# Kernel optimization log

Hardware: AMD Instinct MI355X
Metric: run time of the kernel (lower is better)

## Reference

```python
import jax, jax.numpy as jnp
import numpy as np

EPS = 1e-06
C = 2.0 + EPS

def setup_inputs() -> dict:
    key = jax.random.key(0)
    k1, k2 = jax.random.split(key)
    B, H, D, M, R = 65536, 16, 64, 32, 2
    x = jax.random.normal(k1, (B, H * D), dtype=jnp.float32)
    omega = jax.random.normal(k2, (R, H, D, M), dtype=jnp.float32)
    nodes, weights = np.polynomial.laguerre.laggauss(R)
    quad_nodes = jnp.asarray(nodes, dtype=jnp.float32) / C
    quad_weights = jnp.asarray(weights, dtype=jnp.float32) / C
    return {"x": x, "omega": omega, "quad_nodes": quad_nodes, "quad_weights": quad_weights}

def reference(x, omega, quad_nodes, quad_weights):
    B = x.shape[0]
    R, H, D, M = omega.shape
    inv_sqrt_m = 1.0 / float(M) ** 0.5
    # reshape to heads and normalize each head vector to unit length
    xr = x.reshape(B, H, D)
    norm = jnp.linalg.norm(xr, axis=-1, keepdims=True)
    x_norm = xr / jnp.clip(norm, 1e-06)
    # small projection: contract over head_dim (d=64)
    proj = jnp.einsum('bhd,rhdm->rbhm', x_norm, omega)  # [R,B,H,M]
    poly_feat = proj ** 2 * inv_sqrt_m
    s_vals = quad_nodes.reshape(-1, 1, 1, 1)  # [R,1,1,1]
    sqrt_2s = jnp.sqrt(2.0 * jnp.clip(s_vals, 0.0))
    exp_arg = jnp.clip(proj * sqrt_2s - s_vals, -10.0, 10.0)
    prf_feat = jnp.exp(exp_arg) * inv_sqrt_m
    sq_weights = jnp.sqrt(jnp.clip(quad_weights.reshape(-1, 1, 1, 1), 0.0))
    fused = poly_feat * prf_feat * sq_weights  # [R,B,H,M]
    fused = fused.transpose(1, 2, 0, 3)  # [B,H,R,M]
    return fused.reshape(B, -1)
```

## Files before the change

kernel.cpp:

```cpp
#include <hip/hip_runtime.h>
#include <hip/hip_bf16.h>
#include <math.h>


#define HH 16
#define DD 64
#define MM 32
#define RR 2
#define NN (RR*MM)
#define TILE_B 512
#define NST (TILE_B/64)

using short8  = __attribute__((ext_vector_type(8))) short;
using floatx4 = __attribute__((ext_vector_type(4))) float;

__device__ __forceinline__ short bf16_hi(float v) {
    __hip_bfloat16 b = __float2bfloat16(v);
    return __builtin_bit_cast(short, b);
}
__device__ __forceinline__ float bf16_f(short s) {
    return __uint_as_float(((unsigned)(unsigned short)s) << 16);
}

__global__ __launch_bounds__(256, 5)
void slay_mfma_kernel(const float* __restrict__ x,
                      const float* __restrict__ omega,
                      const float* __restrict__ qn,
                      const float* __restrict__ qw,
                      float* __restrict__ out)
{
    __shared__ short lds_hi[NN * DD];
    __shared__ short lds_lo[NN * DD];
    __shared__ float lds_oc[4][16 * 64];

    const int tid  = threadIdx.x;
    const int lane = tid & 63;
    const int wv   = tid >> 6;
    const int h    = blockIdx.x & (HH - 1);
    const int tile = blockIdx.x >> 4;

    const int mrow = lane & 15;
    const int g    = lane >> 4;

    #pragma unroll
    for (int i = 0; i < (RR * DD * MM) / 256; ++i) {
        int e  = i * 256 + tid;
        int rr = e >> 11;
        int d  = (e >> 5) & (DD - 1);
        int m  = e & (MM - 1);
        float v = omega[((size_t)(rr * HH + h) * DD + d) * MM + m];
        short hi = bf16_hi(v);
        short lo = bf16_hi(v - bf16_f(hi));
        int n   = rr * MM + m;
        int byt = (d * 2) ^ ((n & 7) << 4);
        *(short*)((char*)lds_hi + n * (DD * 2) + byt) = hi;
        *(short*)((char*)lds_lo + n * (DD * 2) + byt) = lo;
    }
    __syncthreads();

    const float sn[2]  = { qn[0], qn[1] };
    const float s2s[2] = { sqrtf(2.f * fmaxf(sn[0], 0.f)), sqrtf(2.f * fmaxf(sn[1], 0.f)) };
    const float cr[2]  = { sqrtf(fmaxf(qw[0], 0.f)) * (1.f / MM),
                           sqrtf(fmaxf(qw[1], 0.f)) * (1.f / MM) };

    const int sw = (mrow & 7) << 4;
    char* const wb = (char*)lds_oc[wv];

    const float* xr0 = x + (size_t)(tile * TILE_B + wv * 16 + mrow) * (HH * DD) + h * DD;

    #pragma unroll
    for (int st = 0; st < NST; ++st) {
        const float* xr = xr0 + (size_t)st * 64 * (HH * DD);
        const int b_base = tile * TILE_B + st * 64 + wv * 16;

        float xv[16];
        *(float4*)(xv + 0)  = *(const float4*)(xr + g * 8);
        *(float4*)(xv + 4)  = *(const float4*)(xr + g * 8 + 4);
        *(float4*)(xv + 8)  = *(const float4*)(xr + 32 + g * 8);
        *(float4*)(xv + 12) = *(const float4*)(xr + 32 + g * 8 + 4);

        float ss = 0.f;
        #pragma unroll
        for (int j = 0; j < 16; ++j) ss = fmaf(xv[j], xv[j], ss);
        ss += __shfl_xor(ss, 16, 64);
        ss += __shfl_xor(ss, 32, 64);
        const float rnorm = 1.0f / fmaxf(sqrtf(ss), 1e-6f);

        short8 x_hi[2], x_lo[2];
        #pragma unroll
        for (int kc = 0; kc < 2; ++kc)
            #pragma unroll
            for (int j = 0; j < 8; ++j) {
                float v  = xv[kc * 8 + j];
                short hi = bf16_hi(v);
                x_hi[kc][j] = hi;
                x_lo[kc][j] = bf16_hi(v - bf16_f(hi));
            }

        #pragma unroll
        for (int nt = 0; nt < 4; ++nt) {
            const char* rh = (const char*)lds_hi + (nt * 16 + mrow) * (DD * 2);
            const char* rl = (const char*)lds_lo + (nt * 16 + mrow) * (DD * 2);
            const int k0 = (g * 16) ^ sw;
            const int k1 = (64 + g * 16) ^ sw;
            short8 oh0 = *(const short8*)(rh + k0);
            short8 oh1 = *(const short8*)(rh + k1);
            short8 ol0 = *(const short8*)(rl + k0);
            short8 ol1 = *(const short8*)(rl + k1);

            floatx4 acc = {0.f, 0.f, 0.f, 0.f};
            acc = __builtin_amdgcn_mfma_f32_16x16x32_bf16(oh0, x_hi[0], acc, 0, 0, 0);
            acc = __builtin_amdgcn_mfma_f32_16x16x32_bf16(oh1, x_hi[1], acc, 0, 0, 0);
            acc = __builtin_amdgcn_mfma_f32_16x16x32_bf16(oh0, x_lo[0], acc, 0, 0, 0);
            acc = __builtin_amdgcn_mfma_f32_16x16x32_bf16(oh1, x_lo[1], acc, 0, 0, 0);
            acc = __builtin_amdgcn_mfma_f32_16x16x32_bf16(ol0, x_hi[0], acc, 0, 0, 0);
            acc = __builtin_amdgcn_mfma_f32_16x16x32_bf16(ol1, x_hi[1], acc, 0, 0, 0);

            const int r = nt >> 1;
            floatx4 res;
            #pragma unroll
            for (int q = 0; q < 4; ++q) {
                float proj = acc[q] * rnorm;
                float ea = fmaf(proj, s2s[r], -sn[r]);
                ea = fminf(fmaxf(ea, -10.f), 10.f);
                res[q] = proj * proj * __expf(ea) * cr[r];
            }
            *(floatx4*)(wb + mrow * 256 + ((nt * 64 + g * 16) ^ sw)) = res;
        }

        #pragma unroll
        for (int i = 0; i < 4; ++i) {
            const int row = i * 4 + g;
            const int col = (mrow) * 16;
            floatx4 v = *(const floatx4*)(wb + row * 256 + (col ^ ((row & 7) << 4)));
            float* op = out + (size_t)(b_base + row) * (HH * NN) + h * NN + mrow * 4;
            __builtin_nontemporal_store(v, (floatx4*)op);
        }
    }
}

extern "C" void kernel_launch(void* const* d_in, const int* in_sizes, int n_in,
                              void* d_out, int out_size, void* d_ws, size_t ws_size,
                              hipStream_t stream) {
    const float* x     = (const float*)d_in[0];
    const float* omega = (const float*)d_in[1];
    const float* qn    = (const float*)d_in[2];
    const float* qw    = (const float*)d_in[3];
    float* out = (float*)d_out;

    const int B = in_sizes[0] / (HH * DD);
    dim3 grid((B / TILE_B) * HH);
    dim3 block(256);

    slay_mfma_kernel<<<grid, block, 0, stream>>>(x, omega, qn, qw, out);
}
```

Measured before the change: 89.47 us.

## Process two heads per block for wider contiguous loads and stores

Each block now handles a pair of adjacent heads instead of one. It stages omega for both heads in LDS and loads 128 contiguous x floats per row. Each output row segment written is 512 bytes instead of 256, which improves coalescing of global reads and writes and halves the grid size. The cost is double the LDS footprint, more registers per thread, and a lower launch_bounds occupancy hint (2 instead of 5), which may reduce latency hiding.

```diff
diff --git a/kernel.cpp b/kernel.cpp
--- a/kernel.cpp
+++ b/kernel.cpp
@@ -22,39 +22,41 @@
     return __uint_as_float(((unsigned)(unsigned short)s) << 16);
 }
 
-__global__ __launch_bounds__(256, 5)
+__global__ __launch_bounds__(256, 2)
 void slay_mfma_kernel(const float* __restrict__ x,
                       const float* __restrict__ omega,
                       const float* __restrict__ qn,
                       const float* __restrict__ qw,
                       float* __restrict__ out)
 {
-    __shared__ short lds_hi[NN * DD];
-    __shared__ short lds_lo[NN * DD];
-    __shared__ float lds_oc[4][16 * 64];
+    __shared__ short lds_hi[2][NN * DD];
+    __shared__ short lds_lo[2][NN * DD];
+    __shared__ float lds_oc[4][16 * 128];
 
     const int tid  = threadIdx.x;
     const int lane = tid & 63;
     const int wv   = tid >> 6;
-    const int h    = blockIdx.x & (HH - 1);
-    const int tile = blockIdx.x >> 4;
+    const int hp   = blockIdx.x & (HH / 2 - 1);
+    const int tile = blockIdx.x >> 3;
+    const int h0   = hp * 2;
 
     const int mrow = lane & 15;
     const int g    = lane >> 4;
 
     #pragma unroll
-    for (int i = 0; i < (RR * DD * MM) / 256; ++i) {
+    for (int i = 0; i < (2 * RR * DD * MM) / 256; ++i) {
         int e  = i * 256 + tid;
-        int rr = e >> 11;
+        int hh = e >> 12;
+        int rr = (e >> 11) & 1;
         int d  = (e >> 5) & (DD - 1);
         int m  = e & (MM - 1);
-        float v = omega[((size_t)(rr * HH + h) * DD + d) * MM + m];
+        float v = omega[((size_t)(rr * HH + h0 + hh) * DD + d) * MM + m];
         short hi = bf16_hi(v);
         short lo = bf16_hi(v - bf16_f(hi));
         int n   = rr * MM + m;
         int byt = (d * 2) ^ ((n & 7) << 4);
-        *(short*)((char*)lds_hi + n * (DD * 2) + byt) = hi;
-        *(short*)((char*)lds_lo + n * (DD * 2) + byt) = lo;
+        *(short*)((char*)lds_hi[hh] + n * (DD * 2) + byt) = hi;
+        *(short*)((char*)lds_lo[hh] + n * (DD * 2) + byt) = lo;
     }
     __syncthreads();
 
@@ -66,74 +68,85 @@
     const int sw = (mrow & 7) << 4;
     char* const wb = (char*)lds_oc[wv];
 
-    const float* xr0 = x + (size_t)(tile * TILE_B + wv * 16 + mrow) * (HH * DD) + h * DD;
+    const float* xr0 = x + (size_t)(tile * TILE_B + wv * 16 + mrow) * (HH * DD) + h0 * DD;
 
     #pragma unroll
     for (int st = 0; st < NST; ++st) {
         const float* xr = xr0 + (size_t)st * 64 * (HH * DD);
         const int b_base = tile * TILE_B + st * 64 + wv * 16;
 
-        float xv[16];
+        float xv[32];
         *(float4*)(xv + 0)  = *(const float4*)(xr + g * 8);
         *(float4*)(xv + 4)  = *(const float4*)(xr + g * 8 + 4);
         *(float4*)(xv + 8)  = *(const float4*)(xr + 32 + g * 8);
         *(float4*)(xv + 12) = *(const float4*)(xr + 32 + g * 8 + 4);
+        *(float4*)(xv + 16) = *(const float4*)(xr + 64 + g * 8);
+        *(float4*)(xv + 20) = *(const float4*)(xr + 64 + g * 8 + 4);
+        *(float4*)(xv + 24) = *(const float4*)(xr + 96 + g * 8);
+        *(float4*)(xv + 28) = *(const float4*)(xr + 96 + g * 8 + 4);
 
-        float ss = 0.f;
+        float rnorm[2];
         #pragma unroll
-        for (int j = 0; j < 16; ++j) ss = fmaf(xv[j], xv[j], ss);
-        ss += __shfl_xor(ss, 16, 64);
-        ss += __shfl_xor(ss, 32, 64);
-        const float rnorm = 1.0f / fmaxf(sqrtf(ss), 1e-6f);
-
-        short8 x_hi[2], x_lo[2];
-        #pragma unroll
-        for (int kc = 0; kc < 2; ++kc)
+        for (int hh = 0; hh < 2; ++hh) {
+            float ss = 0.f;
             #pragma unroll
-            for (int j = 0; j < 8; ++j) {
-                float v  = xv[kc * 8 + j];
-                short hi = bf16_hi(v);
-                x_hi[kc][j] = hi;
-                x_lo[kc][j] = bf16_hi(v - bf16_f(hi));
-            }
-
-        #pragma unroll
-        for (int nt = 0; nt < 4; ++nt) {
-            const char* rh = (const char*)lds_hi + (nt * 16 + mrow) * (DD * 2);
-            const char* rl = (const char*)lds_lo + (nt * 16 + mrow) * (DD * 2);
-            const int k0 = (g * 16) ^ sw;
-            const int k1 = (64 + g * 16) ^ sw;
-            short8 oh0 = *(const short8*)(rh + k0);
-            short8 oh1 = *(const short8*)(rh + k1);
-            short8 ol0 = *(const short8*)(rl + k0);
-            short8 ol1 = *(const short8*)(rl + k1);
-
-            floatx4 acc = {0.f, 0.f, 0.f, 0.f};
-            acc = __builtin_amdgcn_mfma_f32_16x16x32_bf16(oh0, x_hi[0], acc, 0, 0, 0);
-            acc = __builtin_amdgcn_mfma_f32_16x16x32_bf16(oh1, x_hi[1], acc, 0, 0, 0);
-            acc = __builtin_amdgcn_mfma_f32_16x16x32_bf16(oh0, x_lo[0], acc, 0, 0, 0);
-            acc = __builtin_amdgcn_mfma_f32_16x16x32_bf16(oh1, x_lo[1], acc, 0, 0, 0);
-            acc = __builtin_amdgcn_mfma_f32_16x16x32_bf16(ol0, x_hi[0], acc, 0, 0, 0);
-            acc = __builtin_amdgcn_mfma_f32_16x16x32_bf16(ol1, x_hi[1], acc, 0, 0, 0);
-
-            const int r = nt >> 1;
-            floatx4 res;
-            #pragma unroll
-            for (int q = 0; q < 4; ++q) {
-                float proj = acc[q] * rnorm;
-                float ea = fmaf(proj, s2s[r], -sn[r]);
-                ea = fminf(fmaxf(ea, -10.f), 10.f);
-                res[q] = proj * proj * __expf(ea) * cr[r];
-            }
-            *(floatx4*)(wb + mrow * 256 + ((nt * 64 + g * 16) ^ sw)) = res;
+            for (int j = 0; j < 16; ++j) ss = fmaf(xv[hh * 16 + j], xv[hh * 16 + j], ss);
+            ss += __shfl_xor(ss, 16, 64);
+            ss += __shfl_xor(ss, 32, 64);
+            rnorm[hh] = 1.0f / fmaxf(sqrtf(ss), 1e-6f);
         }
 
         #pragma unroll
-        for (int i = 0; i < 4; ++i) {
-            const int row = i * 4 + g;
-            const int col = (mrow) * 16;
-            floatx4 v = *(const floatx4*)(wb + row * 256 + (col ^ ((row & 7) << 4)));
-            float* op = out + (size_t)(b_base + row) * (HH * NN) + h * NN + mrow * 4;
+        for (int hh = 0; hh < 2; ++hh) {
+            short8 x_hi[2], x_lo[2];
+            #pragma unroll
+            for (int kc = 0; kc < 2; ++kc)
+                #pragma unroll
+                for (int j = 0; j < 8; ++j) {
+                    float v  = xv[hh * 16 + kc * 8 + j];
+                    short hi = bf16_hi(v);
+                    x_hi[kc][j] = hi;
+                    x_lo[kc][j] = bf16_hi(v - bf16_f(hi));
+                }
+
+            #pragma unroll
+            for (int nt = 0; nt < 4; ++nt) {
+                const char* rh = (const char*)lds_hi[hh] + (nt * 16 + mrow) * (DD * 2);
+                const char* rl = (const char*)lds_lo[hh] + (nt * 16 + mrow) * (DD * 2);
+                const int k0 = (g * 16) ^ sw;
+                const int k1 = (64 + g * 16) ^ sw;
+                short8 oh0 = *(const short8*)(rh + k0);
+                short8 oh1 = *(const short8*)(rh + k1);
+                short8 ol0 = *(const short8*)(rl + k0);
+                short8 ol1 = *(const short8*)(rl + k1);
+
+                floatx4 acc = {0.f, 0.f, 0.f, 0.f};
+                acc = __builtin_amdgcn_mfma_f32_16x16x32_bf16(oh0, x_hi[0], acc, 0, 0, 0);
+                acc = __builtin_amdgcn_mfma_f32_16x16x32_bf16(oh1, x_hi[1], acc, 0, 0, 0);
+                acc = __builtin_amdgcn_mfma_f32_16x16x32_bf16(oh0, x_lo[0], acc, 0, 0, 0);
+                acc = __builtin_amdgcn_mfma_f32_16x16x32_bf16(oh1, x_lo[1], acc, 0, 0, 0);
+                acc = __builtin_amdgcn_mfma_f32_16x16x32_bf16(ol0, x_hi[0], acc, 0, 0, 0);
+                acc = __builtin_amdgcn_mfma_f32_16x16x32_bf16(ol1, x_hi[1], acc, 0, 0, 0);
+
+                const int r = nt >> 1;
+                floatx4 res;
+                #pragma unroll
+                for (int q = 0; q < 4; ++q) {
+                    float proj = acc[q] * rnorm[hh];
+                    float ea = fmaf(proj, s2s[r], -sn[r]);
+                    ea = fminf(fmaxf(ea, -10.f), 10.f);
+                    res[q] = proj * proj * __expf(ea) * cr[r];
+                }
+                *(floatx4*)(wb + mrow * 512 + ((hh * 256 + nt * 64 + g * 16) ^ sw)) = res;
+            }
+        }
+
+        #pragma unroll
+        for (int i = 0; i < 8; ++i) {
+            const int row  = i * 2 + (lane >> 5);
+            const int colb = (lane & 31) * 16;
+            floatx4 v = *(const floatx4*)(wb + row * 512 + (colb ^ ((row & 7) << 4)));
+            float* op = out + (size_t)(b_base + row) * (HH * NN) + h0 * NN + (lane & 31) * 4;
             __builtin_nontemporal_store(v, (floatx4*)op);
         }
     }
@@ -149,7 +162,7 @@
     float* out = (float*)d_out;
 
     const int B = in_sizes[0] / (HH * DD);
-    dim3 grid((B / TILE_B) * HH);
+    dim3 grid((B / TILE_B) * (HH / 2));
     dim3 block(256);
 
     slay_mfma_kernel<<<grid, block, 0, stream>>>(x, omega, qn, qw, out);
```

New measurement: 91.99 us. 2.8% more time.
